# Kernel tuning notes

Hardware: AMD Instinct MI355X
Metric: run time of the kernel (lower is better)

Reference implementation:

```python
import jax, jax.numpy as jnp
import numpy as np

H = 1024      # hidden_size
HEADS = 1     # heads (must be 1 for the module's einsum->output Linear to type-check)
D = H // HEADS
B = 8
T = 4096
LN_EPS = 1e-5


def setup_inputs() -> dict:
    key = jax.random.key(0)
    ks = jax.random.split(key, 8)
    s = 1.0 / np.sqrt(H)
    return {
        "x": jax.random.normal(ks[0], (B, T, H), dtype=jnp.float32),
        "ln_gamma": jnp.ones((H,), jnp.float32),
        "ln_beta": jnp.zeros((H,), jnp.float32),
        "Wp": jax.random.normal(ks[1], (HEADS + D, H), jnp.float32) * s,  # param_generator weight
        "bp": jnp.zeros((HEADS + D,), jnp.float32),                       # param_generator bias
        "Wg": jax.random.normal(ks[2], (H, H), jnp.float32) * s,          # ghost_update_gate
        "Wt": jax.random.normal(ks[3], (H, H), jnp.float32) * s,          # ghost_update_transform
        "Wr": jax.random.normal(ks[4], (H, H), jnp.float32) * s,          # receptance
        "Wo": jax.random.normal(ks[5], (H, H), jnp.float32) * s,          # output
    }


def reference(x, ln_gamma, ln_beta, Wp, bp, Wg, Wt, Wr, Wo):
    Bb, Tt, Hh = x.shape
    # LayerNorm
    mu = jnp.mean(x, axis=-1, keepdims=True)
    var = jnp.var(x, axis=-1, keepdims=True)
    xn = (x - mu) * jax.lax.rsqrt(var + LN_EPS) * ln_gamma + ln_beta

    r = jnp.einsum('bth,oh->bto', xn, Wr)
    params = jnp.einsum('bth,oh->bto', xn, Wp) + bp
    u = params[..., :HEADS]                                   # [B,T,heads]
    v = params[..., HEADS:]                                   # [B,T,D]

    # active state: cumulative sum of rank-1 outer products u_t v_t^T
    delta_active = u[..., :, None] * v[..., None, :]          # [B,T,heads,D]
    active = jnp.cumsum(delta_active, axis=1)                 # [B,T,heads,D]

    # ghost state: cumulative sum (in fp16, matching ghost_dtype) of gated tanh update
    gate = jax.nn.sigmoid(jnp.einsum('bth,oh->bto', xn, Wg)).reshape(Bb, Tt, HEADS, D)
    trans = jnp.tanh(jnp.einsum('bth,oh->bto', xn,Wt)).reshape(Bb, Tt, HEADS, D)
    ghost = jnp.cumsum((gate * trans).astype(jnp.float16), axis=1)  # [B,T,heads,D] fp16

    combined = active + ghost.astype(active.dtype)
    rt = jax.nn.sigmoid(r).reshape(Bb, Tt, HEADS, D)
    out = jnp.einsum('bthd,bthd->btd', rt, combined)          # sum over heads -> [B,T,D]
    output = jnp.einsum('btd,od->bto', out, Wo)               # [B,T,H] (D==H since heads==1)
    return output, active[:, -1], ghost[:, -1]
```

## Files before the change

kernel.cpp:

```cpp
#include <hip/hip_runtime.h>
#include <cstdint>
#include <cstddef>

#define B_SZ 8
#define T_LEN 4096
#define HD 1024
#define MTOT (B_SZ * T_LEN)

typedef unsigned short u16;
typedef __attribute__((ext_vector_type(8))) short bf16x8;
typedef __attribute__((ext_vector_type(8))) unsigned short us8;
typedef __attribute__((ext_vector_type(4))) float f32x4;
typedef __attribute__((ext_vector_type(16))) float f32x16;

static __device__ __forceinline__ float bf2f(u16 u) {
    union { unsigned i; float f; } v; v.i = ((unsigned)u) << 16; return v.f;
}
static __device__ __forceinline__ u16 f2bf(float f) {
    union { float f; unsigned i; } v; v.f = f;
    unsigned r = v.i + 0x7fffu + ((v.i >> 16) & 1u);
    return (u16)(r >> 16);
}
static __device__ __forceinline__ float sigm(float x) { return 1.f / (1.f + __expf(-x)); }
static __device__ __forceinline__ float tanh_fast(float x) { return 1.f - 2.f / (1.f + __expf(2.f * x)); }
static __device__ __forceinline__ float f4get(const float4& f, int k) {
    return k == 0 ? f.x : k == 1 ? f.y : k == 2 ? f.z : f.w;
}

static __device__ __forceinline__ void gload_lds16(const void* g, void* l) {
    __builtin_amdgcn_global_load_lds((const __attribute__((address_space(1))) void*)g,
                                     (__attribute__((address_space(3))) void*)l, 16, 0, 0);
}

__global__ __launch_bounds__(256) void prep_weights(
    const float* __restrict__ Wp, const float* __restrict__ Wg,
    const float* __restrict__ Wt, const float* __restrict__ Wr,
    const float* __restrict__ Wo, u16* __restrict__ wcat, u16* __restrict__ wob)
{
    int i = blockIdx.x * 256 + threadIdx.x;
    const int T1 = 4096 * 256;
    const int T2 = 1024 * 256;
    if (i < T1) {
        int r = i >> 8, kq = i & 255;
        float4 v;
        if      (r < 1024)  v = ((const float4*)Wp)[(size_t)(r + 1) * 256 + kq];
        else if (r < 2048)  v = ((const float4*)Wg)[(size_t)(r - 1024) * 256 + kq];
        else if (r < 3072)  v = ((const float4*)Wt)[(size_t)(r - 2048) * 256 + kq];
        else                v = ((const float4*)Wr)[(size_t)(r - 3072) * 256 + kq];
        ushort4 o; o.x = f2bf(v.x); o.y = f2bf(v.y); o.z = f2bf(v.z); o.w = f2bf(v.w);
        ((ushort4*)wcat)[i] = o;
    } else if (i < T1 + T2) {
        int j = i - T1;
        float4 v = ((const float4*)Wo)[j];
        ushort4 o; o.x = f2bf(v.x); o.y = f2bf(v.y); o.z = f2bf(v.z); o.w = f2bf(v.w);
        ((ushort4*)wob)[j] = o;
    }
}

__global__ __launch_bounds__(256) void ln_kernel(
    const float* __restrict__ x, const float* __restrict__ gamma,
    const float* __restrict__ beta, const float* __restrict__ Wp,
    const float* __restrict__ bp, u16* __restrict__ xnb, float* __restrict__ u)
{
    __shared__ float red[8];
    const int row = blockIdx.x, tid = threadIdx.x;
    const float4 v = ((const float4*)(x + (size_t)row * HD))[tid];
    float s  = v.x + v.y + v.z + v.w;
    float sq = v.x * v.x + v.y * v.y + v.z * v.z + v.w * v.w;
    #pragma unroll
    for (int off = 32; off > 0; off >>= 1) {
        s  += __shfl_down(s, off);
        sq += __shfl_down(sq, off);
    }
    if ((tid & 63) == 0) { red[tid >> 6] = s; red[4 + (tid >> 6)] = sq; }
    __syncthreads();
    const float S   = red[0] + red[1] + red[2] + red[3];
    const float SQ  = red[4] + red[5] + red[6] + red[7];
    const float mu  = S * (1.f / HD);
    const float var = SQ * (1.f / HD) - mu * mu;
    const float rs  = rsqrtf(var + 1e-5f);
    const float4 gg = ((const float4*)gamma)[tid];
    const float4 bb = ((const float4*)beta)[tid];
    const float x0 = (v.x - mu) * rs * gg.x + bb.x;
    const float x1 = (v.y - mu) * rs * gg.y + bb.y;
    const float x2 = (v.z - mu) * rs * gg.z + bb.z;
    const float x3 = (v.w - mu) * rs * gg.w + bb.w;
    ushort4 o; o.x = f2bf(x0); o.y = f2bf(x1); o.z = f2bf(x2); o.w = f2bf(x3);
    ((ushort4*)(xnb + (size_t)row * HD))[tid] = o;
    const float4 w0 = ((const float4*)Wp)[tid];
    float su = x0 * w0.x + x1 * w0.y + x2 * w0.z + x3 * w0.w;
    #pragma unroll
    for (int off = 32; off > 0; off >>= 1) su += __shfl_down(su, off);
    __syncthreads();
    if ((tid & 63) == 0) red[tid >> 6] = su;
    __syncthreads();
    if (tid == 0) u[row] = red[0] + red[1] + red[2] + red[3] + bp[0];
}

template<int MODE>
__global__ __launch_bounds__(1024, 4) void gemm256(
    const u16* __restrict__ A, const u16* __restrict__ W,
    const float* __restrict__ bp,
    u16* __restrict__ Vt, u16* __restrict__ Gt, u16* __restrict__ Tt, u16* __restrict__ Rt,
    float* __restrict__ Cout)
{
    __shared__ u16 sA[2][256 * 64];
    __shared__ u16 sB[2][256 * 64];
    const int mtile = blockIdx.x, ntile = blockIdx.y;
    const int tid = threadIdx.x;
    const int lane = tid & 63, wave = tid >> 6;
    const int wm = wave >> 2, wn = wave & 3;
    const u16* Ab = A + (size_t)mtile * 256 * 1024;
    const u16* Wb = W + (size_t)ntile * 256 * 1024;

    int goff[2], loff[2];
    #pragma unroll
    for (int jj = 0; jj < 2; ++jj) {
        const int q = jj * 1024 + tid;
        const int r = q >> 3;
        goff[jj] = r * 1024 + ((q & 7) ^ (r & 7)) * 8;
        loff[jj] = q * 8;
    }
    auto stage = [&](int pb, int kt) {
        #pragma unroll
        for (int jj = 0; jj < 2; ++jj) {
            gload_lds16(Ab + goff[jj] + kt * 64, &sA[pb][loff[jj]]);
            gload_lds16(Wb + goff[jj] + kt * 64, &sB[pb][loff[jj]]);
        }
    };

    f32x16 acc[2][2] = {};
    const int rl32  = lane & 31;
    const int khalf = lane >> 5;
    const int sw    = lane & 7;
    const int abase = (wm * 64 + rl32) * 64;
    const int bbase = (wn * 64 + rl32) * 64;

    stage(0, 0);
    for (int t = 0; t < 16; ++t) {
        const int p = t & 1;
        asm volatile("s_waitcnt vmcnt(0)" ::: "memory");
        __builtin_amdgcn_s_barrier();
        __builtin_amdgcn_sched_barrier(0);
        if (t < 15) stage(p ^ 1, t + 1);
        #pragma unroll
        for (int ks = 0; ks < 4; ++ks) {
            const int cs = (ks * 2 + khalf) ^ sw;
            bf16x8 aR[2], bR[2];
            #pragma unroll
            for (int sm = 0; sm < 2; ++sm)
                aR[sm] = *(const bf16x8*)(&sA[p][abase + sm * 2048 + cs * 8]);
            #pragma unroll
            for (int sn = 0; sn < 2; ++sn)
                bR[sn] = *(const bf16x8*)(&sB[p][bbase + sn * 2048 + cs * 8]);
            __builtin_amdgcn_s_setprio(1);
            #pragma unroll
            for (int sm = 0; sm < 2; ++sm)
                #pragma unroll
                for (int sn = 0; sn < 2; ++sn) {
                    if (MODE == 0)
                        acc[sm][sn] = __builtin_amdgcn_mfma_f32_32x32x16_bf16(bR[sn], aR[sm], acc[sm][sn], 0, 0, 0);
                    else
                        acc[sm][sn] = __builtin_amdgcn_mfma_f32_32x32x16_bf16(aR[sm], bR[sn], acc[sm][sn], 0, 0, 0);
                }
            __builtin_amdgcn_s_setprio(0);
        }
    }

    if (MODE == 1) {
        #pragma unroll
        for (int sm = 0; sm < 2; ++sm) {
            #pragma unroll
            for (int sn = 0; sn < 2; ++sn) {
                const int n = ntile * 256 + wn * 64 + sn * 32 + rl32;
                #pragma unroll
                for (int r = 0; r < 16; ++r) {
                    const int m = mtile * 256 + wm * 64 + sm * 32 + (r & 3) + 8 * (r >> 2) + 4 * khalf;
                    Cout[(size_t)m * 1024 + n] = acc[sm][sn][r];
                }
            }
        }
    } else {
        const int seg = ntile >> 2;
        #pragma unroll
        for (int sn = 0; sn < 2; ++sn) {
            #pragma unroll
            for (int r = 0; r < 16; ++r) {
                const int d = (ntile & 3) * 256 + wn * 64 + sn * 32 + (r & 3) + 8 * (r >> 2) + 4 * khalf;
                const size_t drow = (size_t)d * MTOT;
                #pragma unroll
                for (int sm = 0; sm < 2; ++sm) {
                    const int m = mtile * 256 + wm * 64 + sm * 32 + rl32;
                    const float val = acc[sm][sn][r];
                    if (seg == 0) {
                        Vt[drow + m] = f2bf(val + bp[1 + d]);
                    } else if (seg == 1) {
                        Gt[drow + m] = f2bf(sigm(val));
                    } else if (seg == 2) {
                        Tt[drow + m] = f2bf(tanh_fast(val));
                    } else {
                        Rt[drow + m] = f2bf(sigm(val));
                    }
                }
            }
        }
    }
}

__global__ __launch_bounds__(64) void scan_t(
    const u16* __restrict__ Vt, const u16* __restrict__ Gt,
    const u16* __restrict__ Tt, const u16* __restrict__ Rt,
    const float* __restrict__ ub, u16* __restrict__ outb,
    float* __restrict__ act_last, float* __restrict__ gho_last)
{
    const int lane = threadIdx.x;
    const int b  = blockIdx.x >> 4;
    const int d  = ((blockIdx.x & 15) << 6) + lane;
    const int bm0 = b * T_LEN;
    const size_t rbase = (size_t)d * MTOT + bm0;
    const us8* pv = (const us8*)(Vt + rbase);
    const us8* pg = (const us8*)(Gt + rbase);
    const us8* pt = (const us8*)(Tt + rbase);
    const us8* pr = (const us8*)(Rt + rbase);
    const float4* pu = (const float4*)(ub + bm0);

    us8 sv[4][2], sg[4][2], st[4][2], sr[4][2];
    float4 su[4][4];

    #pragma unroll
    for (int c = 0; c < 3; ++c) {
        #pragma unroll
        for (int h = 0; h < 2; ++h) {
            sv[c][h] = pv[c * 2 + h]; sg[c][h] = pg[c * 2 + h];
            st[c][h] = pt[c * 2 + h]; sr[c][h] = pr[c * 2 + h];
        }
        #pragma unroll
        for (int q = 0; q < 4; ++q) su[c][q] = pu[c * 4 + q];
    }

    float acc_a = 0.f;
    _Float16 acc_g = (_Float16)0.f;

    for (int cq = 0; cq < 64; ++cq) {
        #pragma unroll
        for (int s = 0; s < 4; ++s) {
            const int c = cq * 4 + s;
            const int cn = c + 3;
            const int sl = (s + 3) & 3;
            if (cn < 256) {
                #pragma unroll
                for (int h = 0; h < 2; ++h) {
                    sv[sl][h] = pv[cn * 2 + h]; sg[sl][h] = pg[cn * 2 + h];
                    st[sl][h] = pt[cn * 2 + h]; sr[sl][h] = pr[cn * 2 + h];
                }
                #pragma unroll
                for (int q = 0; q < 4; ++q) su[sl][q] = pu[cn * 4 + q];
            }
            #pragma unroll
            for (int e16 = 0; e16 < 16; ++e16) {
                const int h = e16 >> 3, e = e16 & 7;
                const float v  = bf2f(sv[s][h][e]);
                const float g  = bf2f(sg[s][h][e]);
                const float th = bf2f(st[s][h][e]);
                const float r  = bf2f(sr[s][h][e]);
                const float uu = f4get(su[s][e16 >> 2], e16 & 3);
                acc_a = fmaf(uu, v, acc_a);
                acc_g = acc_g + (_Float16)(g * th);
                const float comb = acc_a + (float)acc_g;
                outb[(size_t)(bm0 + c * 16 + e16) * HD + d] = f2bf(r * comb);
            }
        }
    }
    act_last[(size_t)b * HD + d] = acc_a;
    gho_last[(size_t)b * HD + d] = (float)acc_g;
}

extern "C" void kernel_launch(void* const* d_in, const int* in_sizes, int n_in,
                              void* d_out, int out_size, void* d_ws, size_t ws_size,
                              hipStream_t stream)
{
    const float* x   = (const float*)d_in[0];
    const float* gam = (const float*)d_in[1];
    const float* bet = (const float*)d_in[2];
    const float* Wp  = (const float*)d_in[3];
    const float* bp  = (const float*)d_in[4];
    const float* Wg  = (const float*)d_in[5];
    const float* Wt  = (const float*)d_in[6];
    const float* Wr  = (const float*)d_in[7];
    const float* Wo  = (const float*)d_in[8];

    float* out0     = (float*)d_out;
    float* act_last = out0 + (size_t)MTOT * HD;
    float* gho_last = act_last + (size_t)B_SZ * HD;

    char* ws = (char*)d_ws;
    const size_t SZ = (size_t)MTOT * HD * 2;
    u16* xnb  = (u16*)(ws);
    u16* Vt   = (u16*)(ws + SZ);
    u16* Gt   = (u16*)(ws + 2 * SZ);
    u16* Tt   = (u16*)(ws + 3 * SZ);
    u16* Rt   = (u16*)(ws + 4 * SZ);
    u16* wcat = (u16*)(ws + 5 * SZ);
    u16* wob  = (u16*)(ws + 5 * SZ + 8388608);
    float* ub = (float*)(ws + 5 * SZ + 8388608 + 2097152);

    prep_weights<<<5120, 256, 0, stream>>>(Wp, Wg, Wt, Wr, Wo, wcat, wob);
    ln_kernel<<<MTOT, 256, 0, stream>>>(x, gam, bet, Wp, bp, xnb, ub);
    gemm256<0><<<dim3(128, 16), 1024, 0, stream>>>(xnb, wcat, bp, Vt, Gt, Tt, Rt, nullptr);
    scan_t<<<128, 64, 0, stream>>>(Vt, Gt, Tt, Rt, ub, xnb , act_last, gho_last);
    gemm256<1><<<dim3(128, 4), 1024, 0, stream>>>(xnb, wob, bp, nullptr, nullptr, nullptr, nullptr, out0);
}
```

Baseline: 657.2 us.

## Shrink GEMM tiles to 128x256 with K=32 stages and deepen scan prefetch

```diff
diff --git a/kernel.cpp b/kernel.cpp
--- a/kernel.cpp
+++ b/kernel.cpp
@@ -98,61 +98,66 @@
 }
 
 template<int MODE>
-__global__ __launch_bounds__(1024, 4) void gemm256(
+__global__ __launch_bounds__(512, 4) void gemm128x256(
     const u16* __restrict__ A, const u16* __restrict__ W,
     const float* __restrict__ bp,
     u16* __restrict__ Vt, u16* __restrict__ Gt, u16* __restrict__ Tt, u16* __restrict__ Rt,
     float* __restrict__ Cout)
 {
-    __shared__ u16 sA[2][256 * 64];
-    __shared__ u16 sB[2][256 * 64];
+    __shared__ u16 sA[2][128 * 32];
+    __shared__ u16 sB[2][256 * 32];
     const int mtile = blockIdx.x, ntile = blockIdx.y;
     const int tid = threadIdx.x;
     const int lane = tid & 63, wave = tid >> 6;
     const int wm = wave >> 2, wn = wave & 3;
-    const u16* Ab = A + (size_t)mtile * 256 * 1024;
+    const u16* Ab = A + (size_t)mtile * 128 * 1024;
     const u16* Wb = W + (size_t)ntile * 256 * 1024;
 
-    int goff[2], loff[2];
-    #pragma unroll
-    for (int jj = 0; jj < 2; ++jj) {
-        const int q = jj * 1024 + tid;
-        const int r = q >> 3;
-        goff[jj] = r * 1024 + ((q & 7) ^ (r & 7)) * 8;
-        loff[jj] = q * 8;
+    int gA, lA, gB0, lB0, gB1, lB1;
+    {
+        const int q = tid;
+        const int r = q >> 2;
+        gA = r * 1024 + ((q & 3) ^ ((r >> 1) & 3)) * 8;
+        lA = q * 8;
+    }
+    {
+        const int q0 = tid, r0 = q0 >> 2;
+        gB0 = r0 * 1024 + ((q0 & 3) ^ ((r0 >> 1) & 3)) * 8;
+        lB0 = q0 * 8;
+        const int q1 = 512 + tid, r1 = q1 >> 2;
+        gB1 = r1 * 1024 + ((q1 & 3) ^ ((r1 >> 1) & 3)) * 8;
+        lB1 = q1 * 8;
     }
     auto stage = [&](int pb, int kt) {
-        #pragma unroll
-        for (int jj = 0; jj < 2; ++jj) {
-            gload_lds16(Ab + goff[jj] + kt * 64, &sA[pb][loff[jj]]);
-            gload_lds16(Wb + goff[jj] + kt * 64, &sB[pb][loff[jj]]);
-        }
+        gload_lds16(Ab + gA  + kt * 32, &sA[pb][lA]);
+        gload_lds16(Wb + gB0 + kt * 32, &sB[pb][lB0]);
+        gload_lds16(Wb + gB1 + kt * 32, &sB[pb][lB1]);
     };
 
     f32x16 acc[2][2] = {};
     const int rl32  = lane & 31;
     const int khalf = lane >> 5;
-    const int sw    = lane & 7;
-    const int abase = (wm * 64 + rl32) * 64;
-    const int bbase = (wn * 64 + rl32) * 64;
+    const int sw2   = (rl32 >> 1) & 3;
+    const int abase = (wm * 64 + rl32) * 32;
+    const int bbase = (wn * 64 + rl32) * 32;
 
     stage(0, 0);
-    for (int t = 0; t < 16; ++t) {
+    for (int t = 0; t < 32; ++t) {
         const int p = t & 1;
         asm volatile("s_waitcnt vmcnt(0)" ::: "memory");
         __builtin_amdgcn_s_barrier();
         __builtin_amdgcn_sched_barrier(0);
-        if (t < 15) stage(p ^ 1, t + 1);
-        #pragma unroll
-        for (int ks = 0; ks < 4; ++ks) {
-            const int cs = (ks * 2 + khalf) ^ sw;
+        if (t < 31) stage(p ^ 1, t + 1);
+        #pragma unroll
+        for (int ks = 0; ks < 2; ++ks) {
+            const int cs = (ks * 2 + khalf) ^ sw2;
             bf16x8 aR[2], bR[2];
             #pragma unroll
             for (int sm = 0; sm < 2; ++sm)
-                aR[sm] = *(const bf16x8*)(&sA[p][abase + sm * 2048 + cs * 8]);
+                aR[sm] = *(const bf16x8*)(&sA[p][abase + sm * 1024 + cs * 8]);
             #pragma unroll
             for (int sn = 0; sn < 2; ++sn)
-                bR[sn] = *(const bf16x8*)(&sB[p][bbase + sn * 2048 + cs * 8]);
+                bR[sn] = *(const bf16x8*)(&sB[p][bbase + sn * 1024 + cs * 8]);
             __builtin_amdgcn_s_setprio(1);
             #pragma unroll
             for (int sm = 0; sm < 2; ++sm)
@@ -175,7 +180,7 @@
                 const int n = ntile * 256 + wn * 64 + sn * 32 + rl32;
                 #pragma unroll
                 for (int r = 0; r < 16; ++r) {
-                    const int m = mtile * 256 + wm * 64 + sm * 32 + (r & 3) + 8 * (r >> 2) + 4 * khalf;
+                    const int m = mtile * 128 + wm * 64 + sm * 32 + (r & 3) + 8 * (r >> 2) + 4 * khalf;
                     Cout[(size_t)m * 1024 + n] = acc[sm][sn][r];
                 }
             }
@@ -190,7 +195,7 @@
                 const size_t drow = (size_t)d * MTOT;
                 #pragma unroll
                 for (int sm = 0; sm < 2; ++sm) {
-                    const int m = mtile * 256 + wm * 64 + sm * 32 + rl32;
+                    const int m = mtile * 128 + wm * 64 + sm * 32 + rl32;
                     const float val = acc[sm][sn][r];
                     if (seg == 0) {
                         Vt[drow + m] = f2bf(val + bp[1 + d]);
@@ -224,16 +229,19 @@
     const us8* pr = (const us8*)(Rt + rbase);
     const float4* pu = (const float4*)(ub + bm0);
 
-    us8 sv[4][2], sg[4][2], st[4][2], sr[4][2];
+    us8 sv[8][2], sg[8][2], st[8][2], sr[8][2];
     float4 su[4][4];
 
     #pragma unroll
-    for (int c = 0; c < 3; ++c) {
+    for (int c = 0; c < 6; ++c) {
         #pragma unroll
         for (int h = 0; h < 2; ++h) {
             sv[c][h] = pv[c * 2 + h]; sg[c][h] = pg[c * 2 + h];
             st[c][h] = pt[c * 2 + h]; sr[c][h] = pr[c * 2 + h];
         }
+    }
+    #pragma unroll
+    for (int c = 0; c < 3; ++c) {
         #pragma unroll
         for (int q = 0; q < 4; ++q) su[c][q] = pu[c * 4 + q];
     }
@@ -241,21 +249,26 @@
     float acc_a = 0.f;
     _Float16 acc_g = (_Float16)0.f;
 
-    for (int cq = 0; cq < 64; ++cq) {
-        #pragma unroll
-        for (int s = 0; s < 4; ++s) {
-            const int c = cq * 4 + s;
-            const int cn = c + 3;
-            const int sl = (s + 3) & 3;
+    for (int cq = 0; cq < 32; ++cq) {
+        #pragma unroll
+        for (int s = 0; s < 8; ++s) {
+            const int c = cq * 8 + s;
+            const int cn = c + 6;
+            const int sl = (s + 6) & 7;
             if (cn < 256) {
                 #pragma unroll
                 for (int h = 0; h < 2; ++h) {
                     sv[sl][h] = pv[cn * 2 + h]; sg[sl][h] = pg[cn * 2 + h];
                     st[sl][h] = pt[cn * 2 + h]; sr[sl][h] = pr[cn * 2 + h];
                 }
-                #pragma unroll
-                for (int q = 0; q < 4; ++q) su[sl][q] = pu[cn * 4 + q];
-            }
+            }
+            const int cu = c + 3;
+            const int ul = (s + 3) & 3;
+            if (cu < 256) {
+                #pragma unroll
+                for (int q = 0; q < 4; ++q) su[ul][q] = pu[cu * 4 + q];
+            }
+            const int us_ = s & 3;
             #pragma unroll
             for (int e16 = 0; e16 < 16; ++e16) {
                 const int h = e16 >> 3, e = e16 & 7;
@@ -263,7 +276,7 @@
                 const float g  = bf2f(sg[s][h][e]);
                 const float th = bf2f(st[s][h][e]);
                 const float r  = bf2f(sr[s][h][e]);
-                const float uu = f4get(su[s][e16 >> 2], e16 & 3);
+                const float uu = f4get(su[us_][e16 >> 2], e16 & 3);
                 acc_a = fmaf(uu, v, acc_a);
                 acc_g = acc_g + (_Float16)(g * th);
                 const float comb = acc_a + (float)acc_g;
@@ -306,7 +319,7 @@
 
     prep_weights<<<5120, 256, 0, stream>>>(Wp, Wg, Wt, Wr, Wo, wcat, wob);
     ln_kernel<<<MTOT, 256, 0, stream>>>(x, gam, bet, Wp, bp, xnb, ub);
-    gemm256<0><<<dim3(128, 16), 1024, 0, stream>>>(xnb, wcat, bp, Vt, Gt, Tt, Rt, nullptr);
+    gemm128x256<0><<<dim3(256, 16), 512, 0, stream>>>(xnb, wcat, bp, Vt, Gt, Tt, Rt, nullptr);
     scan_t<<<128, 64, 0, stream>>>(Vt, Gt, Tt, Rt, ub, xnb , act_last, gho_last);
-    gemm256<1><<<dim3(128, 4), 1024, 0, stream>>>(xnb, wob, bp, nullptr, nullptr, nullptr, nullptr, out0);
-}
+    gemm128x256<1><<<dim3(256, 4), 512, 0, stream>>>(xnb, wob, bp, nullptr, nullptr, nullptr, nullptr, out0);
+}
```

Measured after the change: 711.8 us. +8.3%, slower.

## Interleave gate/transform weight rows and fuse gated product into GEMM epilogue

Applied to the files above, without the earlier changes.

```diff
diff --git a/kernel.cpp b/kernel.cpp
--- a/kernel.cpp
+++ b/kernel.cpp
@@ -44,8 +44,11 @@
         int r = i >> 8, kq = i & 255;
         float4 v;
         if      (r < 1024)  v = ((const float4*)Wp)[(size_t)(r + 1) * 256 + kq];
-        else if (r < 2048)  v = ((const float4*)Wg)[(size_t)(r - 1024) * 256 + kq];
-        else if (r < 3072)  v = ((const float4*)Wt)[(size_t)(r - 2048) * 256 + kq];
+        else if (r < 3072) {
+            const int d = (r - 1024) >> 1;
+            if (((r - 1024) & 1) == 0) v = ((const float4*)Wg)[(size_t)d * 256 + kq];
+            else                       v = ((const float4*)Wt)[(size_t)d * 256 + kq];
+        }
         else                v = ((const float4*)Wr)[(size_t)(r - 3072) * 256 + kq];
         ushort4 o; o.x = f2bf(v.x); o.y = f2bf(v.y); o.z = f2bf(v.z); o.w = f2bf(v.w);
         ((ushort4*)wcat)[i] = o;
@@ -101,7 +104,7 @@
 __global__ __launch_bounds__(1024, 4) void gemm256(
     const u16* __restrict__ A, const u16* __restrict__ W,
     const float* __restrict__ bp,
-    u16* __restrict__ Vt, u16* __restrict__ Gt, u16* __restrict__ Tt, u16* __restrict__ Rt,
+    u16* __restrict__ Vt, u16* __restrict__ Pt, u16* __restrict__ Rt,
     float* __restrict__ Cout)
 {
     __shared__ u16 sA[2][256 * 64];
@@ -180,8 +183,8 @@
                 }
             }
         }
-    } else {
-        const int seg = ntile >> 2;
+    } else if (ntile < 4 || ntile >= 12) {
+        const bool isV = (ntile < 4);
         #pragma unroll
         for (int sn = 0; sn < 2; ++sn) {
             #pragma unroll
@@ -192,15 +195,26 @@
                 for (int sm = 0; sm < 2; ++sm) {
                     const int m = mtile * 256 + wm * 64 + sm * 32 + rl32;
                     const float val = acc[sm][sn][r];
-                    if (seg == 0) {
-                        Vt[drow + m] = f2bf(val + bp[1 + d]);
-                    } else if (seg == 1) {
-                        Gt[drow + m] = f2bf(sigm(val));
-                    } else if (seg == 2) {
-                        Tt[drow + m] = f2bf(tanh_fast(val));
-                    } else {
-                        Rt[drow + m] = f2bf(sigm(val));
-                    }
+                    if (isV) Vt[drow + m] = f2bf(val + bp[1 + d]);
+                    else     Rt[drow + m] = f2bf(sigm(val));
+                }
+            }
+        }
+    } else {
+        #pragma unroll
+        for (int sn = 0; sn < 2; ++sn) {
+            #pragma unroll
+            for (int j = 0; j < 8; ++j) {
+                const int lrow = (ntile - 4) * 256 + wn * 64 + sn * 32
+                               + ((2 * j) & 3) + 8 * (j >> 1) + 4 * khalf;
+                const int d = lrow >> 1;
+                const size_t drow = (size_t)d * MTOT;
+                #pragma unroll
+                for (int sm = 0; sm < 2; ++sm) {
+                    const int m = mtile * 256 + wm * 64 + sm * 32 + rl32;
+                    union { u16 u; _Float16 h; } pc;
+                    pc.h = (_Float16)(sigm(acc[sm][sn][2 * j]) * tanh_fast(acc[sm][sn][2 * j + 1]));
+                    Pt[drow + m] = pc.u;
                 }
             }
         }
@@ -208,8 +222,8 @@
 }
 
 __global__ __launch_bounds__(64) void scan_t(
-    const u16* __restrict__ Vt, const u16* __restrict__ Gt,
-    const u16* __restrict__ Tt, const u16* __restrict__ Rt,
+    const u16* __restrict__ Vt, const u16* __restrict__ Pt,
+    const u16* __restrict__ Rt,
     const float* __restrict__ ub, u16* __restrict__ outb,
     float* __restrict__ act_last, float* __restrict__ gho_last)
 {
@@ -219,20 +233,18 @@
     const int bm0 = b * T_LEN;
     const size_t rbase = (size_t)d * MTOT + bm0;
     const us8* pv = (const us8*)(Vt + rbase);
-    const us8* pg = (const us8*)(Gt + rbase);
-    const us8* pt = (const us8*)(Tt + rbase);
+    const us8* pp = (const us8*)(Pt + rbase);
     const us8* pr = (const us8*)(Rt + rbase);
     const float4* pu = (const float4*)(ub + bm0);
 
-    us8 sv[4][2], sg[4][2], st[4][2], sr[4][2];
+    us8 sv[4][2], sp[4][2], sr[4][2];
     float4 su[4][4];
 
     #pragma unroll
     for (int c = 0; c < 3; ++c) {
         #pragma unroll
         for (int h = 0; h < 2; ++h) {
-            sv[c][h] = pv[c * 2 + h]; sg[c][h] = pg[c * 2 + h];
-            st[c][h] = pt[c * 2 + h]; sr[c][h] = pr[c * 2 + h];
+            sv[c][h] = pv[c * 2 + h]; sp[c][h] = pp[c * 2 + h]; sr[c][h] = pr[c * 2 + h];
         }
         #pragma unroll
         for (int q = 0; q < 4; ++q) su[c][q] = pu[c * 4 + q];
@@ -250,8 +262,7 @@
             if (cn < 256) {
                 #pragma unroll
                 for (int h = 0; h < 2; ++h) {
-                    sv[sl][h] = pv[cn * 2 + h]; sg[sl][h] = pg[cn * 2 + h];
-                    st[sl][h] = pt[cn * 2 + h]; sr[sl][h] = pr[cn * 2 + h];
+                    sv[sl][h] = pv[cn * 2 + h]; sp[sl][h] = pp[cn * 2 + h]; sr[sl][h] = pr[cn * 2 + h];
                 }
                 #pragma unroll
                 for (int q = 0; q < 4; ++q) su[sl][q] = pu[cn * 4 + q];
@@ -260,12 +271,11 @@
             for (int e16 = 0; e16 < 16; ++e16) {
                 const int h = e16 >> 3, e = e16 & 7;
                 const float v  = bf2f(sv[s][h][e]);
-                const float g  = bf2f(sg[s][h][e]);
-                const float th = bf2f(st[s][h][e]);
                 const float r  = bf2f(sr[s][h][e]);
                 const float uu = f4get(su[s][e16 >> 2], e16 & 3);
+                union { u16 u; _Float16 hh; } pc; pc.u = sp[s][h][e];
                 acc_a = fmaf(uu, v, acc_a);
-                acc_g = acc_g + (_Float16)(g * th);
+                acc_g = acc_g + pc.hh;
                 const float comb = acc_a + (float)acc_g;
                 outb[(size_t)(bm0 + c * 16 + e16) * HD + d] = f2bf(r * comb);
             }
@@ -297,16 +307,15 @@
     const size_t SZ = (size_t)MTOT * HD * 2;
     u16* xnb  = (u16*)(ws);
     u16* Vt   = (u16*)(ws + SZ);
-    u16* Gt   = (u16*)(ws + 2 * SZ);
-    u16* Tt   = (u16*)(ws + 3 * SZ);
-    u16* Rt   = (u16*)(ws + 4 * SZ);
-    u16* wcat = (u16*)(ws + 5 * SZ);
-    u16* wob  = (u16*)(ws + 5 * SZ + 8388608);
-    float* ub = (float*)(ws + 5 * SZ + 8388608 + 2097152);
+    u16* Pt   = (u16*)(ws + 2 * SZ);
+    u16* Rt   = (u16*)(ws + 3 * SZ);
+    u16* wcat = (u16*)(ws + 4 * SZ);
+    u16* wob  = (u16*)(ws + 4 * SZ + 8388608);
+    float* ub = (float*)(ws + 4 * SZ + 8388608 + 2097152);
 
     prep_weights<<<5120, 256, 0, stream>>>(Wp, Wg, Wt, Wr, Wo, wcat, wob);
     ln_kernel<<<MTOT, 256, 0, stream>>>(x, gam, bet, Wp, bp, xnb, ub);
-    gemm256<0><<<dim3(128, 16), 1024, 0, stream>>>(xnb, wcat, bp, Vt, Gt, Tt, Rt, nullptr);
-    scan_t<<<128, 64, 0, stream>>>(Vt, Gt, Tt, Rt, ub, xnb , act_last, gho_last);
-    gemm256<1><<<dim3(128, 4), 1024, 0, stream>>>(xnb, wob, bp, nullptr, nullptr, nullptr, nullptr, out0);
-}
+    gemm256<0><<<dim3(128, 16), 1024, 0, stream>>>(xnb, wcat, bp, Vt, Pt, Rt, nullptr);
+    scan_t<<<128, 64, 0, stream>>>(Vt, Pt, Rt, ub, xnb , act_last, gho_last);
+    gemm256<1><<<dim3(128, 4), 1024, 0, stream>>>(xnb, wob, bp, nullptr, nullptr, nullptr, out0);
+}
```

Result: faster. 589.9 us (-10.2%).
